# Kernel tuning notes

Hardware: AMD Instinct MI355X
Metric: run time of the kernel (lower is better)

Reference implementation:

```python
import jax, jax.numpy as jnp
import numpy as np
from jax import lax

B, C, H, W = 2, 256, 200, 336
N_ROI = 512
NUM_CLASSES = 81


def setup_inputs() -> dict:
    key = jax.random.key(0)
    ks = jax.random.split(key, 20)
    feat = jax.random.normal(ks[0], (B, C, H, W), dtype=jnp.float32)
    # proposals in feature-map coordinates, x1<x2, y1<y2
    x1 = jax.random.uniform(ks[1], (N_ROI,)) * (0.7 * W)
    y1 = jax.random.uniform(ks[2], (N_ROI,)) * (0.7 * H)
    x2 = jnp.minimum(x1 + 8.0 + jax.random.uniform(ks[3], (N_ROI,)) * (0.29 * W), W - 1.0)
    y2 = jnp.minimum(y1 + 8.0 + jax.random.uniform(ks[4], (N_ROI,)) * (0.29 * H), H - 1.0)
    boxes = jnp.stack([x1, y1, x2, y2], axis=1).astype(jnp.float32)
    batch_idx = jax.random.randint(ks[5], (N_ROI,), 0, B)
    s = 0.02
    def rn(k, shape):
        return s * jax.random.normal(k, shape, dtype=jnp.float32)
    d_in = C * 7 * 7  # 12544
    return {
        'feat': feat, 'boxes': boxes,
        'bw1': rn(ks[6], (d_in, 1024)), 'bw2': rn(ks[7], (1024, 1024)), 'bwo': rn(ks[8], (1024, 4 * NUM_CLASSES)),
        'cw1': rn(ks[9], (d_in, 1024)), 'cw2': rn(ks[10], (1024, 1024)), 'cwo': rn(ks[11], (1024, NUM_CLASSES)),
        'm1': rn(ks[12], (C, C, 3, 3)), 'm2': rn(ks[13], (C, C, 3, 3)),
        'm3': rn(ks[14], (C, C, 3, 3)), 'm4': rn(ks[15], (C, C, 3, 3)),
        'mdc': rn(ks[16], (C, C, 2, 2)),  # IOHW for conv_transpose
        'mpr': rn(ks[17], (NUM_CLASSES, C, 1, 1)),
        'batch_idx': batch_idx,
    }


def roi_align(feat, boxes, batch_idx, out_size, sampling_ratio=2):
    """Bilinear RoIAlign. feat [B,C,H,W], boxes [N,4] (x1,y1,x2,y2) in feature coords.
    Returns [N,C,out_size,out_size]."""
    N = boxes.shape[0]
    _, Cc, Hh, Ww = feat.shape
    P = out_size * sampling_ratio
    x1, y1, x2, y2 = boxes[:, 0], boxes[:, 1], boxes[:, 2], boxes[:, 3]
    steps = (jnp.arange(P, dtype=feat.dtype) + 0.5) / P  # [P]
    xs = jnp.clip(x1[:, None] + steps[None, :] * (x2 - x1)[:, None], 0.0, Ww - 1.0)  # [N,P]
    ys = jnp.clip(y1[:, None] + steps[None, :] * (y2 - y1)[:, None], 0.0, Hh - 1.0)  # [N,P]
    x0 = jnp.floor(xs).astype(jnp.int32); x1i = jnp.minimum(x0 + 1, Ww - 1); lx = xs - x0
    y0 = jnp.floor(ys).astype(jnp.int32); y1i = jnp.minimum(y0 + 1, Hh - 1); ly = ys - y0
    b = batch_idx[:, None, None]                   # [N,1,1]
    yy0, yy1 = y0[:, :, None], y1i[:, :, None]     # [N,P,1]
    xx0, xx1 = x0[:, None, :], x1i[:, None, :]     # [N,1,P]
    # gathers -> [N,P,P,C] (advanced indices first, channel slice last)
    f00 = feat[b, :, yy0, xx0]
    f01 = feat[b, :, yy0, xx1]
    f10 = feat[b, :, yy1, xx0]
    f11 = feat[b, :, yy1, xx1]
    wy = ly[:, :, None, None]  # [N,P,1,1]
    wx = lx[:, None, :, None]  # [N,1,P,1]
    val = (f00 * (1 - wy) * (1 - wx) + f01 * (1 - wy) * wx
           + f10 * wy * (1 - wx) + f11 * wy * wx)  # [N,P,P,C]
    pooled = val.reshape(N, out_size, sampling_ratio, out_size, sampling_ratio, Cc).mean(axis=(2, 4))
    return pooled.transpose(0, 3, 1, 2)  # [N,C,out,out]


def _conv(x, w, pad='SAME'):
    return lax.conv_general_dilated(x, w, (1, 1), pad,
                                    dimension_numbers=('NCHW', 'OIHW', 'NCHW'))


def reference(feat, boxes, bw1, bw2, bwo, cw1, cw2, cwo,
              m1, m2, m3, m4, mdc, mpr, batch_idx):
    # RoIAlign (post-NMS proposals) -> box / cls / mask heads
    r7 = roi_align(feat, boxes, batch_idx, 7, 2)          # [N,C,7,7]
    flat = r7.reshape(r7.shape[0], -1)                    # [N, C*49]
    box_result = jax.nn.relu(jax.nn.relu(flat @ bw1) @ bw2) @ bwo   # [N, 4*classes]
    cls_result = jax.nn.relu(jax.nn.relu(flat @ cw1) @ cw2) @ cwo   # [N, classes]
    x = roi_align(feat, boxes, batch_idx, 14, 2)          # [N,C,14,14]
    for w in (m1, m2, m3, m4):
        x = jax.nn.relu(_conv(x, w))
    x = jax.nn.relu(lax.conv_transpose(x, mdc, (2, 2), 'VALID',
                                       dimension_numbers=('NCHW', 'IOHW', 'NCHW')))  # [N,C,28,28]
    mask_result = _conv(x, mpr)                           # [N, classes, 28, 28]
    return (box_result, cls_result, mask_result)
```

## Files before the change

### kernel.cpp

```cpp
#include <hip/hip_runtime.h>
#include <stdint.h>

#define BB 2
#define CC 256
#define HH 200
#define WW 336
#define NROI 512
#define NCLS 81

typedef __attribute__((ext_vector_type(8))) short bf16x8;
typedef __attribute__((ext_vector_type(4))) float f32x4;

__device__ inline unsigned short f2bf(float f) {
  unsigned int u = __builtin_bit_cast(unsigned int, f);
  u += 0x7fffu + ((u >> 16) & 1u);
  return (unsigned short)(u >> 16);
}
__device__ inline float bf2f(unsigned short h) {
  unsigned int u = ((unsigned int)h) << 16;
  return __builtin_bit_cast(float, u);
}

__device__ inline void gl_lds(const void* gp, void* lp) {
  __builtin_amdgcn_global_load_lds(
      (const __attribute__((address_space(1))) unsigned int*)gp,
      (__attribute__((address_space(3))) unsigned int*)lp, 16, 0, 0);
}

__global__ void k_nchw2nhwc(const float* __restrict__ src, unsigned short* __restrict__ dst) {
  __shared__ float t[32][33];
  int b = blockIdx.z;
  int p0 = blockIdx.x * 32;
  int c0 = blockIdx.y * 32;
  int tx = threadIdx.x & 31, ty = threadIdx.x >> 5;
  const float* s = src + (size_t)b * CC * HH * WW;
  unsigned short* d = dst + (size_t)b * CC * HH * WW;
#pragma unroll
  for (int q = 0; q < 4; ++q)
    t[ty + q * 8][tx] = s[(size_t)(c0 + ty + q * 8) * (HH * WW) + p0 + tx];
  __syncthreads();
#pragma unroll
  for (int q = 0; q < 4; ++q)
    d[(size_t)(p0 + ty + q * 8) * CC + c0 + tx] = f2bf(t[tx][ty + q * 8]);
}

__global__ void k_repack_convw4(const float* __restrict__ w0, const float* __restrict__ w1,
                                const float* __restrict__ w2, const float* __restrict__ w3,
                                unsigned short* __restrict__ wT) {
  int d = blockIdx.x * 256 + threadIdx.x;
  if (d >= 589824) return;
  int which = blockIdx.y;
  const float* w = (which == 0) ? w0 : (which == 1) ? w1 : (which == 2) ? w2 : w3;
  int c = d & 255, o = (d >> 8) & 255, t = d >> 16;
  wT[(size_t)which * 589824 + d] = f2bf(w[o * 2304 + c * 9 + t]);
}

__global__ void k_repack_deconv(const float* __restrict__ mdc, unsigned short* __restrict__ wd) {
  int d = blockIdx.x * 256 + threadIdx.x;
  if (d >= 262144) return;
  int c = d & 255, o = (d >> 8) & 255, tap = d >> 16;
  int r = tap >> 1, s = tap & 1;
  wd[d] = f2bf(mdc[c * 1024 + o * 4 + (1 - r) * 2 + (1 - s)]);
}

__global__ void k_repack_mpr(const float* __restrict__ mpr, unsigned short* __restrict__ mT) {
  int d = blockIdx.x * 256 + threadIdx.x;
  if (d >= 32768) return;
  int c = d & 255, o = d >> 8;
  mT[d] = (o < 81) ? f2bf(mpr[o * 256 + c]) : (unsigned short)0;
}

__global__ void k_repack_w1(const float* __restrict__ src, unsigned short* __restrict__ dst) {
  __shared__ float t[32][33];
  int s = blockIdx.x;
  int c0 = blockIdx.y * 32;
  int n0 = blockIdx.z * 32;
  int tx = threadIdx.x & 31, ty = threadIdx.x >> 5;
#pragma unroll
  for (int q = 0; q < 4; ++q)
    t[ty + q * 8][tx] = src[(size_t)((c0 + ty + q * 8) * 49 + s) * 1024 + n0 + tx];
  __syncthreads();
#pragma unroll
  for (int q = 0; q < 4; ++q)
    dst[(size_t)(n0 + ty + q * 8) * 12544 + s * 256 + c0 + tx] = f2bf(t[tx][ty + q * 8]);
}

__global__ void k_transpose_w(const float* __restrict__ src, unsigned short* __restrict__ dst,
                              int K, int Nreal, int Nphys) {
  __shared__ float t[32][33];
  int k0 = blockIdx.x * 32;
  int n0 = blockIdx.y * 32;
  int tx = threadIdx.x & 31, ty = threadIdx.x >> 5;
#pragma unroll
  for (int q = 0; q < 4; ++q) {
    int n = n0 + tx;
    t[ty + q * 8][tx] = (n < Nreal) ? src[(size_t)(k0 + ty + q * 8) * Nreal + n] : 0.f;
  }
  __syncthreads();
#pragma unroll
  for (int q = 0; q < 4; ++q) {
    int n = n0 + ty + q * 8;
    if (n < Nphys) dst[(size_t)n * K + k0 + tx] = f2bf(t[tx][ty + q * 8]);
  }
}

__global__ void k_zero_border(unsigned short* __restrict__ r14p,
                              unsigned short* __restrict__ cbufA,
                              unsigned short* __restrict__ cbufB) {
  unsigned short* base = (blockIdx.y == 0) ? r14p : (blockIdx.y == 1) ? cbufA : cbufB;
  uint4 z = {0u, 0u, 0u, 0u};
#pragma unroll
  for (int q = 0; q < 8; ++q) {
    int lin = blockIdx.x * 2048 + q * 256 + threadIdx.x;
    int row = lin >> 5, u4 = lin & 31;
    int img = row / 60, b = row - img * 60;
    int y, x;
    if (b < 16) { y = 0; x = b; }
    else if (b < 32) { y = 15; x = b - 16; }
    else { int rem = b - 32; y = 1 + (rem >> 1); x = (rem & 1) * 15; }
    int slot = img * 256 + y * 16 + x;
    ((uint4*)base)[(size_t)slot * 32 + u4] = z;
  }
}

template <int OS>
__global__ void k_roialign(const unsigned short* __restrict__ featN, const float* __restrict__ boxes,
                           const int* __restrict__ bidx, unsigned short* __restrict__ out) {
  const int S = OS * OS;
  int blk = blockIdx.x;
  int n = blk / S;
  int s = blk - n * S;
  int oy = s / OS, ox = s - oy * OS;
  int c = threadIdx.x;
  float x1 = boxes[n * 4 + 0], y1 = boxes[n * 4 + 1];
  float x2 = boxes[n * 4 + 2], y2 = boxes[n * 4 + 3];
  const unsigned short* fb = featN + (size_t)bidx[n] * HH * WW * CC;
  const float P = (float)(OS * 2);
  float acc = 0.f;
#pragma unroll
  for (int sy = 0; sy < 2; ++sy)
#pragma unroll
    for (int sx = 0; sx < 2; ++sx) {
      float xs = x1 + ((float)(ox * 2 + sx) + 0.5f) / P * (x2 - x1);
      float ys = y1 + ((float)(oy * 2 + sy) + 0.5f) / P * (y2 - y1);
      xs = fminf(fmaxf(xs, 0.f), (float)(WW - 1));
      ys = fminf(fmaxf(ys, 0.f), (float)(HH - 1));
      int x0 = (int)floorf(xs);
      int y0 = (int)floorf(ys);
      int x1i = min(x0 + 1, WW - 1);
      int y1i = min(y0 + 1, HH - 1);
      float lx = xs - (float)x0, ly = ys - (float)y0;
      float f00 = bf2f(fb[((y0 * WW + x0) << 8) + c]);
      float f01 = bf2f(fb[((y0 * WW + x1i) << 8) + c]);
      float f10 = bf2f(fb[((y1i * WW + x0) << 8) + c]);
      float f11 = bf2f(fb[((y1i * WW + x1i) << 8) + c]);
      acc += f00 * (1.f - ly) * (1.f - lx) + f01 * (1.f - ly) * lx +
             f10 * ly * (1.f - lx) + f11 * ly * lx;
    }
  acc *= 0.25f;
  if (OS == 7) {
    out[(size_t)n * 12544 + s * 256 + c] = f2bf(acc);
  } else {
    int slot = n * 256 + (oy + 1) * 16 + (ox + 1);
    out[((size_t)slot << 8) + c] = f2bf(acc);
  }
}

#define TM 128
#define TN 128
#define TK 32

__global__ __launch_bounds__(256) void k_gemm_bf16(
    const unsigned short* __restrict__ A0, const unsigned short* __restrict__ Bt0, void* __restrict__ O0p,
    const unsigned short* __restrict__ A1, const unsigned short* __restrict__ Bt1, void* __restrict__ O1p,
    int K, int Nreal, int ldO, int mode, int relu, int ki, int kj) {
  const unsigned short* A = blockIdx.z ? A1 : A0;
  const unsigned short* Bt = blockIdx.z ? Bt1 : Bt0;
  void* Op = blockIdx.z ? O1p : O0p;

  __shared__ unsigned short As[TM * TK];
  __shared__ unsigned short Bs[TN * TK];

  int tid = threadIdx.x, lane = tid & 63, w = tid >> 6;
  int m0 = blockIdx.y * TM, n0 = blockIdx.x * TN;
  int lr = lane >> 2, lc = (lane & 3) * 8;

  const unsigned short* aP[2];
  const unsigned short* bP[2];
  unsigned short* asL[2];
  unsigned short* bsL[2];
#pragma unroll
  for (int s = 0; s < 2; ++s) {
    int seg = w * 2 + s;
    aP[s] = A + (size_t)(m0 + seg * 16 + lr) * K + lc;
    bP[s] = Bt + (size_t)(n0 + seg * 16 + lr) * K + lc;
    asL[s] = As + seg * 512;
    bsL[s] = Bs + seg * 512;
  }

  f32x4 acc[4][4] = {};
  int wm = (w & 1) * 64, wn = (w >> 1) * 64;
  int qa = (lane >> 4) * 8, rl = lane & 15;

  for (int k0 = 0; k0 < K; k0 += TK) {
    gl_lds(aP[0], asL[0]);
    gl_lds(aP[1], asL[1]);
    gl_lds(bP[0], bsL[0]);
    gl_lds(bP[1], bsL[1]);
    aP[0] += TK; aP[1] += TK; bP[0] += TK; bP[1] += TK;
    __syncthreads();
    bf16x8 af[4], bfr[4];
#pragma unroll
    for (int i = 0; i < 4; ++i)
      af[i] = *(const bf16x8*)&As[(wm + i * 16 + rl) * TK + qa];
#pragma unroll
    for (int j = 0; j < 4; ++j)
      bfr[j] = *(const bf16x8*)&Bs[(wn + j * 16 + rl) * TK + qa];
#pragma unroll
    for (int i = 0; i < 4; ++i)
#pragma unroll
      for (int j = 0; j < 4; ++j)
        acc[i][j] = __builtin_amdgcn_mfma_f32_16x16x32_bf16(af[i], bfr[j], acc[i][j], 0, 0, 0);
    __syncthreads();
  }

  int col = lane & 15, rquad = (lane >> 4) * 4;
#pragma unroll
  for (int i = 0; i < 4; ++i) {
#pragma unroll
    for (int j = 0; j < 4; ++j) {
      int gn = n0 + wn + j * 16 + col;
#pragma unroll
      for (int r = 0; r < 4; ++r) {
        int gm = m0 + wm + i * 16 + rquad + r;
        float v = acc[i][j][r];
        if (relu) v = fmaxf(v, 0.f);
        if (mode == 0) {
          ((unsigned short*)Op)[(size_t)gm * ldO + gn] = f2bf(v);
        } else if (mode == 1) {
          if (gn < Nreal) ((float*)Op)[(size_t)gm * ldO + gn] = v;
        } else {
          if (gn < Nreal) {
            int nimg = gm / 196;
            int s2 = gm - nimg * 196;
            int ii = s2 / 14, jj = s2 - ii * 14;
            size_t dst = (((size_t)nimg * 81 + gn) * 28 + (2 * ii + ki)) * 28 + (2 * jj + kj);
            ((float*)Op)[dst] = v;
          }
        }
      }
    }
  }
}

__global__ __launch_bounds__(256) void k_fc1(
    const unsigned short* __restrict__ A, const unsigned short* __restrict__ Bb,
    const unsigned short* __restrict__ Bc, float* __restrict__ Opart) {
  int head = blockIdx.z >> 3, slice = blockIdx.z & 7;
  const unsigned short* Bt = head ? Bc : Bb;

  __shared__ unsigned short As[TM * TK];
  __shared__ unsigned short Bs[TN * TK];

  int tid = threadIdx.x, lane = tid & 63, w = tid >> 6;
  int m0 = blockIdx.y * TM, n0 = blockIdx.x * TN;
  int lr = lane >> 2, lc = (lane & 3) * 8;
  int kbase = slice * 1568;

  const unsigned short* aP[2];
  const unsigned short* bP[2];
  unsigned short* asL[2];
  unsigned short* bsL[2];
#pragma unroll
  for (int s = 0; s < 2; ++s) {
    int seg = w * 2 + s;
    aP[s] = A + (size_t)(m0 + seg * 16 + lr) * 12544 + kbase + lc;
    bP[s] = Bt + (size_t)(n0 + seg * 16 + lr) * 12544 + kbase + lc;
    asL[s] = As + seg * 512;
    bsL[s] = Bs + seg * 512;
  }

  f32x4 acc[4][4] = {};
  int wm = (w & 1) * 64, wn = (w >> 1) * 64;
  int qa = (lane >> 4) * 8, rl = lane & 15;

  for (int k0 = 0; k0 < 1568; k0 += TK) {
    gl_lds(aP[0], asL[0]);
    gl_lds(aP[1], asL[1]);
    gl_lds(bP[0], bsL[0]);
    gl_lds(bP[1], bsL[1]);
    aP[0] += TK; aP[1] += TK; bP[0] += TK; bP[1] += TK;
    __syncthreads();
    bf16x8 af[4], bfr[4];
#pragma unroll
    for (int i = 0; i < 4; ++i)
      af[i] = *(const bf16x8*)&As[(wm + i * 16 + rl) * TK + qa];
#pragma unroll
    for (int j = 0; j < 4; ++j)
      bfr[j] = *(const bf16x8*)&Bs[(wn + j * 16 + rl) * TK + qa];
#pragma unroll
    for (int i = 0; i < 4; ++i)
#pragma unroll
      for (int j = 0; j < 4; ++j)
        acc[i][j] = __builtin_amdgcn_mfma_f32_16x16x32_bf16(af[i], bfr[j], acc[i][j], 0, 0, 0);
    __syncthreads();
  }

  float* O = Opart + (size_t)(head * 8 + slice) * 524288;
  int col = lane & 15, rquad = (lane >> 4) * 4;
#pragma unroll
  for (int i = 0; i < 4; ++i)
#pragma unroll
    for (int j = 0; j < 4; ++j) {
      int gn = n0 + wn + j * 16 + col;
#pragma unroll
      for (int r = 0; r < 4; ++r) {
        int gm = m0 + wm + i * 16 + rquad + r;
        O[(size_t)gm * 1024 + gn] = acc[i][j][r];
      }
    }
}

__global__ void k_fc1red(const float* __restrict__ part, unsigned short* __restrict__ h1b,
                         unsigned short* __restrict__ h1c) {
  int head = blockIdx.y;
  int i = blockIdx.x * 256 + threadIdx.x;
  const float* p = part + (size_t)head * 8 * 524288 + i;
  float s = 0.f;
#pragma unroll
  for (int q = 0; q < 8; ++q) s += p[(size_t)q * 524288];
  unsigned short* h = head ? h1c : h1b;
  h[i] = f2bf(fmaxf(s, 0.f));
}

template <int PADOUT>
__global__ __launch_bounds__(256) void k_conv3m(const unsigned short* __restrict__ act,
                                                const unsigned short* __restrict__ wt,
                                                unsigned short* __restrict__ out) {
  __shared__ unsigned short As[TM * TK];
  __shared__ unsigned short Bs[TN * TK];

  int tid = threadIdx.x, lane = tid & 63, w = tid >> 6;
  int m0 = blockIdx.y * TM, n0 = blockIdx.x * TN;
  int lr = lane >> 2, lc = (lane & 3) * 8;

  const unsigned short* aB[2];
  const unsigned short* bB[2];
  unsigned short* asL[2];
  unsigned short* bsL[2];
#pragma unroll
  for (int s = 0; s < 2; ++s) {
    int seg = w * 2 + s;
    int m = m0 + seg * 16 + lr;
    int n = m / 196;
    int rem = m - n * 196;
    int y = rem / 14, x = rem - y * 14;
    int slot = n * 256 + (y + 1) * 16 + (x + 1);
    aB[s] = act + ((size_t)slot << 8) + lc;
    bB[s] = wt + (size_t)(n0 + seg * 16 + lr) * 256 + lc;
    asL[s] = As + seg * 512;
    bsL[s] = Bs + seg * 512;
  }

  f32x4 acc[4][4] = {};
  int wm = (w & 1) * 64, wn = (w >> 1) * 64;
  int qa = (lane >> 4) * 8, rl = lane & 15;

  for (int ky = -1; ky <= 1; ++ky) {
    for (int kx = -1; kx <= 1; ++kx) {
      int aoff = (ky * 16 + kx) * 256;
      int boff = ((ky + 1) * 3 + (kx + 1)) * 65536;
      for (int c0 = 0; c0 < 256; c0 += TK) {
        gl_lds(aB[0] + aoff + c0, asL[0]);
        gl_lds(aB[1] + aoff + c0, asL[1]);
        gl_lds(bB[0] + boff + c0, bsL[0]);
        gl_lds(bB[1] + boff + c0, bsL[1]);
        __syncthreads();
        bf16x8 af[4], bfr[4];
#pragma unroll
        for (int i = 0; i < 4; ++i)
          af[i] = *(const bf16x8*)&As[(wm + i * 16 + rl) * TK + qa];
#pragma unroll
        for (int j = 0; j < 4; ++j)
          bfr[j] = *(const bf16x8*)&Bs[(wn + j * 16 + rl) * TK + qa];
#pragma unroll
        for (int i = 0; i < 4; ++i)
#pragma unroll
          for (int j = 0; j < 4; ++j)
            acc[i][j] = __builtin_amdgcn_mfma_f32_16x16x32_bf16(af[i], bfr[j], acc[i][j], 0, 0, 0);
        __syncthreads();
      }
    }
  }

  int col = lane & 15, rquad = (lane >> 4) * 4;
#pragma unroll
  for (int i = 0; i < 4; ++i) {
#pragma unroll
    for (int r = 0; r < 4; ++r) {
      int gm = m0 + wm + i * 16 + rquad + r;
      size_t rowbase;
      if (PADOUT) {
        int n = gm / 196;
        int rem = gm - n * 196;
        int y = rem / 14, x = rem - y * 14;
        rowbase = ((size_t)(n * 256 + (y + 1) * 16 + (x + 1))) << 8;
      } else {
        rowbase = (size_t)gm << 8;
      }
#pragma unroll
      for (int j = 0; j < 4; ++j) {
        int gn = n0 + wn + j * 16 + col;
        out[rowbase + gn] = f2bf(fmaxf(acc[i][j][r], 0.f));
      }
    }
  }
}

extern "C" void kernel_launch(void* const* d_in, const int* in_sizes, int n_in,
                              void* d_out, int out_size, void* d_ws, size_t ws_size,
                              hipStream_t stream) {
  (void)in_sizes; (void)n_in; (void)out_size; (void)ws_size;
  const float* feat = (const float*)d_in[0];
  const float* boxes = (const float*)d_in[1];
  const float* bw1 = (const float*)d_in[2];
  const float* bw2 = (const float*)d_in[3];
  const float* bwo = (const float*)d_in[4];
  const float* cw1 = (const float*)d_in[5];
  const float* cw2 = (const float*)d_in[6];
  const float* cwo = (const float*)d_in[7];
  const float* m1 = (const float*)d_in[8];
  const float* m2 = (const float*)d_in[9];
  const float* m3 = (const float*)d_in[10];
  const float* m4 = (const float*)d_in[11];
  const float* mdc = (const float*)d_in[12];
  const float* mpr = (const float*)d_in[13];
  const int* bidx = (const int*)d_in[14];

  char* p = (char*)d_ws;
  unsigned short* featN = (unsigned short*)p; p += 68812800;
  unsigned short* cbufA = featN;
  unsigned short* cbufB = (unsigned short*)p; p += 67108864;
  float* fc1part = (float*)cbufB;
  unsigned short* r14p = (unsigned short*)p;  p += 67108864;
  unsigned short* dflat = (unsigned short*)p; p += 51380224;
  unsigned short* ddec = (unsigned short*)p;  p += 51380224;
  unsigned short* r7b = (unsigned short*)p;   p += 12845056;
  unsigned short* h1b = (unsigned short*)p;   p += 1048576;
  unsigned short* h1c = (unsigned short*)p;   p += 1048576;
  unsigned short* h2b = (unsigned short*)p;   p += 1048576;
  unsigned short* h2c = (unsigned short*)p;   p += 1048576;
  unsigned short* wTb = (unsigned short*)p;   p += 4718592;
  unsigned short* wdb = (unsigned short*)p;   p += 524288;
  unsigned short* mprTb = (unsigned short*)p; p += 65536;
  unsigned short* bw1b = (unsigned short*)p;  p += 25690112;
  unsigned short* cw1b = (unsigned short*)p;  p += 25690112;
  unsigned short* bw2b = (unsigned short*)p;  p += 2097152;
  unsigned short* cw2b = (unsigned short*)p;  p += 2097152;
  unsigned short* bwob = (unsigned short*)p;  p += 786432;
  unsigned short* cwob = (unsigned short*)p;  p += 262144;

  float* outBox = (float*)d_out;
  float* outCls = outBox + 512 * 324;
  float* outMask = outCls + 512 * 81;

  k_nchw2nhwc<<<dim3(2100, 8, 2), 256, 0, stream>>>(feat, featN);
  k_repack_convw4<<<dim3(2304, 4), 256, 0, stream>>>(m1, m2, m3, m4, wTb);
  k_repack_deconv<<<dim3(1024), 256, 0, stream>>>(mdc, wdb);
  k_repack_mpr<<<dim3(128), 256, 0, stream>>>(mpr, mprTb);
  k_repack_w1<<<dim3(49, 8, 32), 256, 0, stream>>>(bw1, bw1b);
  k_repack_w1<<<dim3(49, 8, 32), 256, 0, stream>>>(cw1, cw1b);
  k_transpose_w<<<dim3(32, 32), 256, 0, stream>>>(bw2, bw2b, 1024, 1024, 1024);
  k_transpose_w<<<dim3(32, 32), 256, 0, stream>>>(cw2, cw2b, 1024, 1024, 1024);
  k_transpose_w<<<dim3(32, 12), 256, 0, stream>>>(bwo, bwob, 1024, 324, 384);
  k_transpose_w<<<dim3(32, 4), 256, 0, stream>>>(cwo, cwob, 1024, 81, 128);

  k_roialign<7><<<dim3(512 * 49), 256, 0, stream>>>(featN, boxes, bidx, r7b);
  k_roialign<14><<<dim3(512 * 196), 256, 0, stream>>>(featN, boxes, bidx, r14p);

  k_fc1<<<dim3(8, 4, 16), 256, 0, stream>>>(r7b, bw1b, cw1b, fc1part);
  k_fc1red<<<dim3(2048, 2), 256, 0, stream>>>(fc1part, h1b, h1c);
  k_gemm_bf16<<<dim3(8, 4, 2), 256, 0, stream>>>(h1b, bw2b, h2b, h1c, cw2b, h2c,
                                                 1024, 1024, 1024, 0, 1, 0, 0);
  k_gemm_bf16<<<dim3(3, 4, 1), 256, 0, stream>>>(h2b, bwob, outBox, h2b, bwob, outBox,
                                                 1024, 324, 324, 1, 0, 0, 0);
  k_gemm_bf16<<<dim3(1, 4, 1), 256, 0, stream>>>(h2c, cwob, outCls, h2c, cwob, outCls,
                                                 1024, 81, 81, 1, 0, 0, 0);

  k_zero_border<<<dim3(480, 3), 256, 0, stream>>>(r14p, cbufA, cbufB);
  k_conv3m<1><<<dim3(2, 784), 256, 0, stream>>>(r14p, wTb + 0 * 589824, cbufA);
  k_conv3m<1><<<dim3(2, 784), 256, 0, stream>>>(cbufA, wTb + 1 * 589824, cbufB);
  k_conv3m<1><<<dim3(2, 784), 256, 0, stream>>>(cbufB, wTb + 2 * 589824, cbufA);
  k_conv3m<0><<<dim3(2, 784), 256, 0, stream>>>(cbufA, wTb + 3 * 589824, dflat);

  for (int r = 0; r < 2; ++r)
    for (int s = 0; s < 2; ++s) {
      int tap = r * 2 + s;
      k_gemm_bf16<<<dim3(2, 784, 1), 256, 0, stream>>>(
          dflat, wdb + tap * 65536, ddec, dflat, wdb, ddec,
          256, 256, 256, 0, 1, 0, 0);
      k_gemm_bf16<<<dim3(1, 784, 1), 256, 0, stream>>>(
          ddec, mprTb, outMask, ddec, mprTb, outMask,
          256, 81, 0, 2, 0, r, s);
    }
}
```

Before: 1.748 ms.

## Rewrite mask-head 3x3 conv as 256x256-tile double-buffered swizzled MFMA kernel

Replaces the 128x128-tile conv kernel (2x784 blocks, 256 threads, single LDS buffer with two barriers per K step) with a 256x256 tile kernel using 512 threads and K=64 stages. It double-buffers global-to-LDS loads so the next tap/channel stage loads while MFMAs run, XOR-swizzles the LDS layout to avoid bank conflicts, remaps blocks across M, and raises wave priority around MFMA blocks. This cuts redundant activation reloads (the full N=256 now fits in one block) and barrier stalls. The cost is higher register use (32 accumulators per lane), 128KB of LDS per block, and only 392 blocks, which may limit occupancy.

```diff
diff --git a/kernel.cpp b/kernel.cpp
--- a/kernel.cpp
+++ b/kernel.cpp
@@ -334,71 +334,90 @@
 }
 
 template <int PADOUT>
-__global__ __launch_bounds__(256) void k_conv3m(const unsigned short* __restrict__ act,
-                                                const unsigned short* __restrict__ wt,
-                                                unsigned short* __restrict__ out) {
-  __shared__ unsigned short As[TM * TK];
-  __shared__ unsigned short Bs[TN * TK];
-
-  int tid = threadIdx.x, lane = tid & 63, w = tid >> 6;
-  int m0 = blockIdx.y * TM, n0 = blockIdx.x * TN;
-  int lr = lane >> 2, lc = (lane & 3) * 8;
-
-  const unsigned short* aB[2];
-  const unsigned short* bB[2];
-  unsigned short* asL[2];
-  unsigned short* bsL[2];
-#pragma unroll
-  for (int s = 0; s < 2; ++s) {
-    int seg = w * 2 + s;
-    int m = m0 + seg * 16 + lr;
-    int n = m / 196;
-    int rem = m - n * 196;
+__global__ __launch_bounds__(512, 2) void k_conv256(const unsigned short* __restrict__ act,
+                                                    const unsigned short* __restrict__ wt,
+                                                    unsigned short* __restrict__ out) {
+  __shared__ unsigned short As[2][16384];
+  __shared__ unsigned short Bs[2][16384];
+
+  int tid = threadIdx.x, lane = tid & 63, wv = tid >> 6;
+  int mt = (blockIdx.x & 7) * 49 + (blockIdx.x >> 3);
+  int m0 = mt * 256;
+
+  int r8 = tid >> 3;
+  int j8 = ((tid & 7) ^ (r8 & 7)) * 8;
+  int slotA[4];
+  int bElem[4];
+#pragma unroll
+  for (int q = 0; q < 4; ++q) {
+    int row = q * 64 + r8;
+    int gm = m0 + row;
+    int n = gm / 196;
+    int rem = gm - n * 196;
     int y = rem / 14, x = rem - y * 14;
-    int slot = n * 256 + (y + 1) * 16 + (x + 1);
-    aB[s] = act + ((size_t)slot << 8) + lc;
-    bB[s] = wt + (size_t)(n0 + seg * 16 + lr) * 256 + lc;
-    asL[s] = As + seg * 512;
-    bsL[s] = Bs + seg * 512;
-  }
-
-  f32x4 acc[4][4] = {};
-  int wm = (w & 1) * 64, wn = (w >> 1) * 64;
-  int qa = (lane >> 4) * 8, rl = lane & 15;
-
-  for (int ky = -1; ky <= 1; ++ky) {
-    for (int kx = -1; kx <= 1; ++kx) {
-      int aoff = (ky * 16 + kx) * 256;
-      int boff = ((ky + 1) * 3 + (kx + 1)) * 65536;
-      for (int c0 = 0; c0 < 256; c0 += TK) {
-        gl_lds(aB[0] + aoff + c0, asL[0]);
-        gl_lds(aB[1] + aoff + c0, asL[1]);
-        gl_lds(bB[0] + boff + c0, bsL[0]);
-        gl_lds(bB[1] + boff + c0, bsL[1]);
-        __syncthreads();
-        bf16x8 af[4], bfr[4];
-#pragma unroll
-        for (int i = 0; i < 4; ++i)
-          af[i] = *(const bf16x8*)&As[(wm + i * 16 + rl) * TK + qa];
-#pragma unroll
-        for (int j = 0; j < 4; ++j)
-          bfr[j] = *(const bf16x8*)&Bs[(wn + j * 16 + rl) * TK + qa];
-#pragma unroll
-        for (int i = 0; i < 4; ++i)
-#pragma unroll
-          for (int j = 0; j < 4; ++j)
-            acc[i][j] = __builtin_amdgcn_mfma_f32_16x16x32_bf16(af[i], bfr[j], acc[i][j], 0, 0, 0);
-        __syncthreads();
-      }
+    slotA[q] = n * 256 + (y + 1) * 16 + (x + 1);
+    bElem[q] = row * 256 + j8;
+  }
+  int ldsU = wv * 512;
+
+  int wr = wv >> 2, wc = wv & 3;
+  int rl = lane & 15, lg = lane >> 4, e = lane & 7;
+  int swz0 = ((lg) ^ e) * 8;
+  int swz1 = ((4 + lg) ^ e) * 8;
+
+  f32x4 acc[8][4] = {};
+
+#define STAGE(S, D)                                                               \
+  do {                                                                            \
+    int cb_ = (S) / 9;                                                            \
+    int t_ = (S) - cb_ * 9;                                                       \
+    int ky_ = t_ / 3, kx_ = t_ - ky_ * 3;                                         \
+    int tapd_ = (ky_ - 1) * 16 + (kx_ - 1);                                       \
+    int coff_ = cb_ * 64;                                                         \
+    _Pragma("unroll") for (int q = 0; q < 4; ++q)                                 \
+        gl_lds(act + (size_t)(slotA[q] + tapd_) * 256 + coff_ + j8,               \
+               &As[D][q * 4096 + ldsU]);                                          \
+    _Pragma("unroll") for (int q = 0; q < 4; ++q)                                 \
+        gl_lds(wt + (size_t)t_ * 65536 + bElem[q] + coff_,                        \
+               &Bs[D][q * 4096 + ldsU]);                                          \
+  } while (0)
+
+  STAGE(0, 0);
+  __syncthreads();
+
+  for (int s = 0; s < 36; ++s) {
+    int cur = s & 1;
+    if (s + 1 < 36) STAGE(s + 1, cur ^ 1);
+    const unsigned short* Ab = As[cur];
+    const unsigned short* Bb = Bs[cur];
+#pragma unroll
+    for (int ks = 0; ks < 2; ++ks) {
+      int sw = ks ? swz1 : swz0;
+      bf16x8 a[8], b[4];
+#pragma unroll
+      for (int fi = 0; fi < 8; ++fi)
+        a[fi] = *(const bf16x8*)&Ab[(wr * 128 + fi * 16 + rl) * 64 + sw];
+#pragma unroll
+      for (int fj = 0; fj < 4; ++fj)
+        b[fj] = *(const bf16x8*)&Bb[(wc * 64 + fj * 16 + rl) * 64 + sw];
+      __builtin_amdgcn_s_setprio(1);
+#pragma unroll
+      for (int fi = 0; fi < 8; ++fi)
+#pragma unroll
+        for (int fj = 0; fj < 4; ++fj)
+          acc[fi][fj] = __builtin_amdgcn_mfma_f32_16x16x32_bf16(a[fi], b[fj], acc[fi][fj], 0, 0, 0);
+      __builtin_amdgcn_s_setprio(0);
     }
-  }
-
-  int col = lane & 15, rquad = (lane >> 4) * 4;
-#pragma unroll
-  for (int i = 0; i < 4; ++i) {
+    __syncthreads();
+  }
+#undef STAGE
+
+  int col = lane & 15, rquad = lg * 4;
+#pragma unroll
+  for (int fi = 0; fi < 8; ++fi) {
 #pragma unroll
     for (int r = 0; r < 4; ++r) {
-      int gm = m0 + wm + i * 16 + rquad + r;
+      int gm = m0 + wr * 128 + fi * 16 + rquad + r;
       size_t rowbase;
       if (PADOUT) {
         int n = gm / 196;
@@ -409,9 +428,9 @@
         rowbase = (size_t)gm << 8;
       }
 #pragma unroll
-      for (int j = 0; j < 4; ++j) {
-        int gn = n0 + wn + j * 16 + col;
-        out[rowbase + gn] = f2bf(fmaxf(acc[i][j][r], 0.f));
+      for (int fj = 0; fj < 4; ++fj) {
+        int gn = wc * 64 + fj * 16 + col;
+        out[rowbase + gn] = f2bf(fmaxf(acc[fi][fj][r], 0.f));
       }
     }
   }
@@ -488,10 +507,10 @@
                                                  1024, 81, 81, 1, 0, 0, 0);
 
   k_zero_border<<<dim3(480, 3), 256, 0, stream>>>(r14p, cbufA, cbufB);
-  k_conv3m<1><<<dim3(2, 784), 256, 0, stream>>>(r14p, wTb + 0 * 589824, cbufA);
-  k_conv3m<1><<<dim3(2, 784), 256, 0, stream>>>(cbufA, wTb + 1 * 589824, cbufB);
-  k_conv3m<1><<<dim3(2, 784), 256, 0, stream>>>(cbufB, wTb + 2 * 589824, cbufA);
-  k_conv3m<0><<<dim3(2, 784), 256, 0, stream>>>(cbufA, wTb + 3 * 589824, dflat);
+  k_conv256<1><<<dim3(392), 512, 0, stream>>>(r14p, wTb + 0 * 589824, cbufA);
+  k_conv256<1><<<dim3(392), 512, 0, stream>>>(cbufA, wTb + 1 * 589824, cbufB);
+  k_conv256<1><<<dim3(392), 512, 0, stream>>>(cbufB, wTb + 2 * 589824, cbufA);
+  k_conv256<0><<<dim3(392), 512, 0, stream>>>(cbufA, wTb + 3 * 589824, dflat);
 
   for (int r = 0; r < 2; ++r)
     for (int s = 0; s < 2; ++s) {
```

New measurement: 1.677 ms. 1.04x faster.
